# Kernel tuning notes

Hardware: AMD Instinct MI355X
Metric: run time of the kernel (lower is better)

Reference implementation:

```python
import jax, jax.numpy as jnp
import numpy as np

H, DH, C, K = 8, 128, 200, 15  # heads, head_dim, context_size, conv kernel
SCALE = DH ** -0.5
EPS = 1e-5


def layernorm(x, g, b):
    mu = jnp.mean(x, axis=-1, keepdims=True)
    var = jnp.mean(jnp.square(x - mu), axis=-1, keepdims=True)
    return (x - mu) * jax.lax.rsqrt(var + EPS) * g + b


def feedforward(x, ln_g, ln_b, up_w, up_b, down_w, down_b):
    h = layernorm(x, ln_g, ln_b)
    h = jax.nn.silu(h @ up_w + up_b)
    return h @ down_w + down_b


def attention(x, dist, ln_g, ln_b, wq, wkv, wo, wo_b, rel_emb):
    h = layernorm(x, ln_g, ln_b)
    b, f, d = h.shape
    nb = f // C  # num_features chosen divisible by context_size (no remainder path)
    q = (h @ wq).reshape(b, nb, C, H, DH).transpose(0, 1, 3, 2, 4)   # [b,nb,H,C,dh]
    kv = h @ wkv
    k, v = jnp.split(kv, 2, axis=-1)
    k = k.reshape(b, nb, C, H, DH).transpose(0, 1, 3, 2, 4)
    v = v.reshape(b, nb, C, H, DH).transpose(0, 1, 3, 2, 4)
    rel = rel_emb[dist]                                              # [C,C,dh]
    pos_attn = jnp.einsum('bnhid,ijd->bnhij', q, rel) * SCALE
    scores = jnp.einsum('bnhid,bnhjd->bnhij', q, k) * SCALE + pos_attn
    probs = jax.nn.softmax(scores, axis=-1)
    out = jnp.einsum('bnhij,bnhjd->bnhid', probs, v)
    out = out.transpose(0, 1, 3, 2, 4).reshape(b, f, H * DH)
    return out @ wo + wo_b


def conv_module(x, ln_g, ln_b, up_w, up_b, dw_w, bn_g, bn_b, bn_mean, bn_var, down_w, down_b):
    h = layernorm(x, ln_g, ln_b)
    h = h @ up_w + up_b                         # pointwise conv == linear; [b,L,2*inner]
    a, gate = jnp.split(h, 2, axis=-1)
    h = a * jax.nn.sigmoid(gate)                # GLU over channel dim
    h = h.transpose(0, 2, 1)                    # [b,inner,L]
    pad = K // 2
    h = jax.lax.conv_general_dilated(
        h, dw_w[:, None, :], window_strides=(1,), padding=[(pad, pad)],
        dimension_numbers=('NCH', 'OIH', 'NCH'), feature_group_count=h.shape[1])
    # BatchNorm1d in eval mode (running stats)
    h = (h - bn_mean[None, :, None]) * jax.lax.rsqrt(bn_var[None, :, None] + EPS)
    h = h * bn_g[None, :, None] + bn_b[None, :, None]
    h = jax.nn.silu(h)
    h = h.transpose(0, 2, 1) @ down_w + down_b  # [b,L,hidden]
    return h


def block_forward(x, attention_dists,
                  ff1_ln_g, ff1_ln_b, ff1_up_w, ff1_up_b, ff1_down_w, ff1_down_b,
                  attn_ln_g, attn_ln_b, wq, wkv, wo, wo_b, rel_emb,
                  conv_ln_g, conv_ln_b, conv_up_w, conv_up_b, dw_w,
                  bn_g, bn_b, bn_mean, bn_var, conv_down_w, conv_down_b,
                  ff2_ln_g, ff2_ln_b, ff2_up_w, ff2_up_b, ff2_down_w, ff2_down_b,
                  post_ln_g, post_ln_b):
    x = 0.5 * feedforward(x, ff1_ln_g, ff1_ln_b, ff1_up_w, ff1_up_b, ff1_down_w, ff1_down_b) + x
    x = attention(x, attention_dists, attn_ln_g, attn_ln_b, wq, wkv, wo, wo_b, rel_emb) + x
    x = conv_module(x, conv_ln_g, conv_ln_b, conv_up_w, conv_up_b, dw_w,
                    bn_g, bn_b, bn_mean, bn_var, conv_down_w, conv_down_b) + x
    x = 0.5 * feedforward(x, ff2_ln_g, ff2_ln_b, ff2_up_w, ff2_up_b, ff2_down_w, ff2_down_b) + x
    return layernorm(x, post_ln_g, post_ln_b)


def setup_inputs() -> dict:
    key = jax.random.key(0)
    ks = iter(jax.random.split(key, 40))
    d, dff, inner = 1024, 4096, 2048
    r = lambda shape, s=0.02: (jax.random.normal(next(ks), shape, jnp.float32) * s)
    inp = {
        'x': jax.random.normal(next(ks), (8, 2000, d), jnp.float32),
        'attention_dists': jax.random.randint(next(ks), (C, C), 0, 1025, jnp.int32),
        'ff1_ln_g': jnp.ones((d,)), 'ff1_ln_b': jnp.zeros((d,)),
        'ff1_up_w': r((d, dff)), 'ff1_up_b': jnp.zeros((dff,)),
        'ff1_down_w': r((dff, d)), 'ff1_down_b': jnp.zeros((d,)),
        'attn_ln_g': jnp.ones((d,)), 'attn_ln_b': jnp.zeros((d,)),
        'wq': r((d, H * DH)), 'wkv': r((d, 2 * H * DH)),
        'wo': r((H * DH, d)), 'wo_b': jnp.zeros((d,)),
        'rel_emb': r((2 * 512 + 1, DH)),
        'conv_ln_g': jnp.ones((d,)), 'conv_ln_b': jnp.zeros((d,)),
        'conv_up_w': r((d, 2 * inner)), 'conv_up_b': jnp.zeros((2 * inner,)),
        'dw_w': r((inner, K)),
        'bn_g': jnp.ones((inner,)), 'bn_b': jnp.zeros((inner,)),
        'bn_mean': r((inner,)), 'bn_var': jax.random.uniform(next(ks), (inner,), jnp.float32) + 0.5,
        'conv_down_w': r((inner, d)), 'conv_down_b': jnp.zeros((d,)),
        'ff2_ln_g': jnp.ones((d,)), 'ff2_ln_b': jnp.zeros((d,)),
        'ff2_up_w': r((d, dff)), 'ff2_up_b': jnp.zeros((dff,)),
        'ff2_down_w': r((dff, d)), 'ff2_down_b': jnp.zeros((d,)),
        'post_ln_g': jnp.ones((d,)), 'post_ln_b': jnp.zeros((d,)),
    }
    return inp


def reference(x, attention_dists,
              ff1_ln_g, ff1_ln_b, ff1_up_w, ff1_up_b, ff1_down_w, ff1_down_b,
              attn_ln_g, attn_ln_b, wq, wkv, wo, wo_b, rel_emb,
              conv_ln_g, conv_ln_b, conv_up_w, conv_up_b, dw_w,
              bn_g, bn_b, bn_mean, bn_var, conv_down_w, conv_down_b,
              ff2_ln_g, ff2_ln_b, ff2_up_w, ff2_up_b, ff2_down_w, ff2_down_b,
              post_ln_g, post_ln_b):
    return block_forward(x, attention_dists,
                         ff1_ln_g, ff1_ln_b, ff1_up_w, ff1_up_b, ff1_down_w, ff1_down_b,
                         attn_ln_g, attn_ln_b, wq, wkv, wo, wo_b, rel_emb,
                         conv_ln_g, conv_ln_b, conv_up_w, conv_up_b, dw_w,
                         bn_g, bn_b, bn_mean, bn_var, conv_down_w, conv_down_b,
                         ff2_ln_g, ff2_ln_b, ff2_up_w, ff2_up_b, ff2_down_w, ff2_down_b,
                         post_ln_g, post_ln_b)
```

## Files before the change

### kernel.cpp

```cpp
#include <hip/hip_runtime.h>

typedef unsigned short u16;
typedef unsigned int u32;
using short8 = __attribute__((ext_vector_type(8))) short;
using floatx4 = __attribute__((ext_vector_type(4))) float;

#define DMODEL 1024
#define DFF 4096
#define INNER 2048
#define DH 128
#define CTX 200
#define R_TOT 16000
#define ABN 40
#define AROWS (ABN * CTX)
#define AM (ABN * 8)
#define SCALE_Q 0.08838834764831845f

__device__ __forceinline__ u16 f2bf(float f) {
    union { float f; u32 u; } v; v.f = f;
    u32 r = v.u + 0x7FFFu + ((v.u >> 16) & 1u);
    return (u16)(r >> 16);
}
__device__ __forceinline__ float bf2f(u16 u) {
    union { u32 u; float f; } v; v.u = ((u32)u) << 16; return v.f;
}
__device__ __forceinline__ float sigmoidf_(float x) { return 1.f / (1.f + __expf(-x)); }

__device__ __forceinline__ void load_lds16(const void* g, void* l) {
    __builtin_amdgcn_global_load_lds((const __attribute__((address_space(1))) u32*)g,
                                     (__attribute__((address_space(3))) u32*)l, 16, 0, 0);
}

__device__ __forceinline__ void xcd_stripe_remap(int& bx, int& by) {
    const int gx = gridDim.x;
    const int gxs = gx >> 3;
    const int id = blockIdx.y * gx + blockIdx.x;
    const int xcd = id & 7;
    const int local = id >> 3;
    bx = xcd * gxs + (local % gxs);
    by = local / gxs;
}

template <int MODE>
__device__ __forceinline__ void epi_store(int r, int c, float v, int M, int ldc,
                                          const float* bias, float alpha, void* out,
                                          const float* resid) {
    if (r >= M) return;
    size_t idx = (size_t)r * ldc + c;
    float bb = bias ? bias[c] : 0.f;
    if (MODE == 0) {
        ((u16*)out)[idx] = f2bf(alpha * v + bb);
    } else if (MODE == 1) {
        float t = v + bb;
        ((u16*)out)[idx] = f2bf(t * sigmoidf_(t));
    } else {
        ((float*)out)[idx] = alpha * (v + bb) + resid[idx];
    }
}

template <int MODE>
__global__ __launch_bounds__(256, 4) void k_g(const u16* __restrict__ A, int lda,
                                              const u16* __restrict__ Bt, int ldb,
                                              const float* __restrict__ bias, float alpha,
                                              void* out, int ldc, const float* resid, int M,
                                              int N, int K) {
    __shared__ __align__(128) char lds[32768];
    int bx, by;
    xcd_stripe_remap(bx, by);
    const int row0 = bx * 128, col0 = by * 128;
    if (row0 >= M) return;
    const int lane = threadIdx.x & 63;
    const int wave = threadIdx.x >> 6;
    const int wrow = (wave >> 1) * 64;
    const int wcol = (wave & 1) * 64;
    const int lr = lane & 15;
    const int kg = lane >> 4;
    const int nt = K >> 6;

    const char* sA[4];
    const char* sB[4];
#pragma unroll
    for (int r = 0; r < 4; ++r) {
        int o = r * 4096 + wave * 1024 + lane * 16;
        int row = o >> 7;
        int srcb = (o & 127) ^ ((row & 7) << 4);
        int ga = row0 + row;
        ga = (ga < M) ? ga : M - 1;
        sA[r] = (const char*)A + (size_t)ga * ((size_t)lda * 2) + srcb;
        int gb = col0 + row;
        gb = (gb < N) ? gb : N - 1;
        sB[r] = (const char*)Bt + (size_t)gb * ((size_t)ldb * 2) + srcb;
    }
    floatx4 acc[4][4];
#pragma unroll
    for (int i = 0; i < 4; ++i)
#pragma unroll
        for (int j = 0; j < 4; ++j) acc[i][j] = (floatx4){0.f, 0.f, 0.f, 0.f};

    for (int t = 0; t < nt; ++t) {
        const int kb = t << 7;
#pragma unroll
        for (int r = 0; r < 4; ++r) {
            load_lds16(sA[r] + kb, lds + r * 4096 + wave * 1024);
            load_lds16(sB[r] + kb, lds + 16384 + r * 4096 + wave * 1024);
        }
        asm volatile("s_waitcnt vmcnt(0)" ::: "memory");
        __builtin_amdgcn_s_barrier();
#pragma unroll
        for (int ks = 0; ks < 2; ++ks) {
            short8 av[4], bv[4];
#pragma unroll
            for (int mi = 0; mi < 4; ++mi) {
                int row = wrow + mi * 16 + lr;
                int cb = (ks * 64 + kg * 16) ^ ((row & 7) << 4);
                av[mi] = *(const short8*)(lds + row * 128 + cb);
            }
#pragma unroll
            for (int ni = 0; ni < 4; ++ni) {
                int row = wcol + ni * 16 + lr;
                int cb = (ks * 64 + kg * 16) ^ ((row & 7) << 4);
                bv[ni] = *(const short8*)(lds + 16384 + row * 128 + cb);
            }
#pragma unroll
            for (int mi = 0; mi < 4; ++mi)
#pragma unroll
                for (int ni = 0; ni < 4; ++ni)
                    acc[mi][ni] = __builtin_amdgcn_mfma_f32_16x16x32_bf16(av[mi], bv[ni],
                                                                          acc[mi][ni], 0, 0, 0);
        }
        asm volatile("s_waitcnt lgkmcnt(0)" ::: "memory");
        __builtin_amdgcn_s_barrier();
    }
#pragma unroll
    for (int mi = 0; mi < 4; ++mi)
#pragma unroll
        for (int ni = 0; ni < 4; ++ni)
#pragma unroll
            for (int rr = 0; rr < 4; ++rr)
                epi_store<MODE>(row0 + wrow + mi * 16 + kg * 4 + rr, col0 + wcol + ni * 16 + lr,
                                acc[mi][ni][rr], M, ldc, bias, alpha, out, resid);
}

template <typename RowMap>
__device__ __forceinline__ void stage_tile_s(const char* __restrict__ src, RowMap rowoff,
                                             int nrows, int row0, int k0b, char* tile) {
    const int lane = threadIdx.x & 63;
    const int wave = threadIdx.x >> 6;
#pragma unroll
    for (int r = 0; r < 4; ++r) {
        int o = r * 4096 + wave * 1024 + lane * 16;
        int row = o >> 7;
        int srcb = (o & 127) ^ ((row & 7) << 4);
        int grow = row0 + row;
        grow = (grow < nrows) ? grow : (nrows - 1);
        load_lds16(src + rowoff(grow) + k0b + srcb, tile + r * 4096 + wave * 1024);
    }
}

template <typename RMA, typename RMB, typename Epi>
__device__ __forceinline__ void gemm_core_s(const char* __restrict__ A, RMA rma, int a_rows,
                                            const char* __restrict__ B, RMB rmb, int b_rows,
                                            int K, int row0, int col0, char* lds, Epi epi) {
    const int lane = threadIdx.x & 63;
    const int wave = threadIdx.x >> 6;
    const int wrow = (wave >> 1) * 64;
    const int wcol = (wave & 1) * 64;
    const int lr = lane & 15;
    const int kg = lane >> 4;
    const int nt = K >> 6;

    floatx4 acc[4][4];
#pragma unroll
    for (int i = 0; i < 4; ++i)
#pragma unroll
        for (int j = 0; j < 4; ++j) acc[i][j] = (floatx4){0.f, 0.f, 0.f, 0.f};

    for (int t = 0; t < nt; ++t) {
        const int kb = t << 7;
        stage_tile_s(A, rma, a_rows, row0, kb, lds);
        stage_tile_s(B, rmb, b_rows, col0, kb, lds + 16384);
        asm volatile("s_waitcnt vmcnt(0)" ::: "memory");
        __builtin_amdgcn_s_barrier();
#pragma unroll
        for (int ks = 0; ks < 2; ++ks) {
            short8 av[4], bv[4];
#pragma unroll
            for (int mi = 0; mi < 4; ++mi) {
                int row = wrow + mi * 16 + lr;
                int cb = (ks * 64 + kg * 16) ^ ((row & 7) << 4);
                av[mi] = *(const short8*)(lds + row * 128 + cb);
            }
#pragma unroll
            for (int ni = 0; ni < 4; ++ni) {
                int row = wcol + ni * 16 + lr;
                int cb = (ks * 64 + kg * 16) ^ ((row & 7) << 4);
                bv[ni] = *(const short8*)(lds + 16384 + row * 128 + cb);
            }
#pragma unroll
            for (int mi = 0; mi < 4; ++mi)
#pragma unroll
                for (int ni = 0; ni < 4; ++ni)
                    acc[mi][ni] = __builtin_amdgcn_mfma_f32_16x16x32_bf16(av[mi], bv[ni],
                                                                          acc[mi][ni], 0, 0, 0);
        }
        asm volatile("s_waitcnt lgkmcnt(0)" ::: "memory");
        __builtin_amdgcn_s_barrier();
    }
#pragma unroll
    for (int mi = 0; mi < 4; ++mi)
#pragma unroll
        for (int ni = 0; ni < 4; ++ni)
#pragma unroll
            for (int rr = 0; rr < 4; ++rr)
                epi(row0 + wrow + mi * 16 + kg * 4 + rr, col0 + wcol + ni * 16 + lr,
                    acc[mi][ni][rr]);
}

__global__ __launch_bounds__(256, 4) void k_qk(const u16* __restrict__ q,
                                               const u16* __restrict__ kvc,
                                               u16* __restrict__ sc, int bn0) {
    __shared__ __align__(128) char lds[32768];
    const int z = blockIdx.z, bnl = z >> 3, h = z & 7;
    const char* A = (const char*)(q + ((size_t)(bn0 + bnl) * CTX) * DMODEL + h * DH);
    const char* B = (const char*)(kvc + ((size_t)bnl * CTX) * (2 * DMODEL) + h * DH);
    u16* out = sc + (size_t)z * CTX * 256;
    gemm_core_s(A, [](int r) { return (size_t)r * (DMODEL * 2); }, CTX, B,
                [](int r) { return (size_t)r * (4 * DMODEL); }, CTX, DH, blockIdx.x * 128,
                blockIdx.y * 128, lds, [&](int r, int c, float v) {
                    if (r < CTX) out[(size_t)r * 256 + c] = f2bf(v);
                });
}

__global__ __launch_bounds__(256, 4) void k_pos(const u16* __restrict__ q,
                                                const u16* __restrict__ rel,
                                                u16* __restrict__ sc, int m0) {
    __shared__ __align__(128) char lds[32768];
    const int i = blockIdx.z;
    const char* B = (const char*)(rel + (size_t)i * CTX * DH);
    u16* out = sc + i * 256;
    gemm_core_s((const char*)q,
                [=](int r) {
                    int m = m0 + r;
                    return (size_t)(((m >> 3) * CTX + i) * DMODEL + (m & 7) * DH) * 2;
                },
                AM, B, [](int r) { return (size_t)r * (DH * 2); }, CTX, DH, blockIdx.x * 128,
                blockIdx.y * 128, lds, [&](int r, int c, float v) {
                    if (r < AM) {
                        size_t idx = (size_t)r * (CTX * 256) + c;
                        out[idx] = f2bf(bf2f(out[idx]) + v);
                    }
                });
}

__global__ __launch_bounds__(256, 4) void k_pv(const u16* __restrict__ P,
                                               const u16* __restrict__ vT,
                                               u16* __restrict__ attn, int bn0) {
    __shared__ __align__(128) char lds[32768];
    const int z = blockIdx.z;
    u16* out = attn + ((size_t)(bn0 + (z >> 3)) * CTX) * DMODEL + (z & 7) * DH;
    const char* A = (const char*)(P + (size_t)z * CTX * 256);
    const char* B = (const char*)(vT + (size_t)z * DH * 256);
    gemm_core_s(A, [](int r) { return (size_t)r * 512; }, CTX, B,
                [](int r) { return (size_t)r * 512; }, DH, 256, blockIdx.x * 128, 0, lds,
                [&](int r, int c, float v) {
                    if (r < CTX) out[(size_t)r * DMODEL + c] = f2bf(v);
                });
}

template <bool OUTF32>
__global__ __launch_bounds__(256) void k_ln(const float* __restrict__ x,
                                            const float* __restrict__ g,
                                            const float* __restrict__ b, void* __restrict__ out) {
    const int row = blockIdx.x, t = threadIdx.x, lane = t & 63, wv = t >> 6;
    const float4 v = ((const float4*)(x + (size_t)row * DMODEL))[t];
    float s = v.x + v.y + v.z + v.w;
    float q = v.x * v.x + v.y * v.y + v.z * v.z + v.w * v.w;
#pragma unroll
    for (int off = 32; off > 0; off >>= 1) { s += __shfl_down(s, off); q += __shfl_down(q, off); }
    __shared__ float rs_[4], rq_[4];
    if (lane == 0) { rs_[wv] = s; rq_[wv] = q; }
    __syncthreads();
    s = rs_[0] + rs_[1] + rs_[2] + rs_[3];
    q = rq_[0] + rq_[1] + rq_[2] + rq_[3];
    const float mu = s * (1.f / DMODEL);
    const float rstd = rsqrtf(q * (1.f / DMODEL) - mu * mu + 1e-5f);
    const float4 gv = ((const float4*)g)[t];
    const float4 bv = ((const float4*)b)[t];
    float o0 = (v.x - mu) * rstd * gv.x + bv.x;
    float o1 = (v.y - mu) * rstd * gv.y + bv.y;
    float o2 = (v.z - mu) * rstd * gv.z + bv.z;
    float o3 = (v.w - mu) * rstd * gv.w + bv.w;
    if (OUTF32) {
        ((float4*)out)[(size_t)row * 256 + t] = make_float4(o0, o1, o2, o3);
    } else {
        ushort4 r4;
        r4.x = f2bf(o0); r4.y = f2bf(o1); r4.z = f2bf(o2); r4.w = f2bf(o3);
        ((ushort4*)out)[(size_t)row * 256 + t] = r4;
    }
}

__global__ __launch_bounds__(256) void k_softmax(u16* __restrict__ sc) {
    const size_t row = blockIdx.x;
    const int t = threadIdx.x, lane = t & 63, wv = t >> 6;
    float v = (t < CTX) ? bf2f(sc[row * 256 + t]) : -3.0e38f;
    float m = v;
#pragma unroll
    for (int off = 32; off > 0; off >>= 1) m = fmaxf(m, __shfl_down(m, off));
    __shared__ float rm[4], rsum[4];
    if (lane == 0) rm[wv] = m;
    __syncthreads();
    m = fmaxf(fmaxf(rm[0], rm[1]), fmaxf(rm[2], rm[3]));
    float e = (t < CTX) ? __expf(v - m) : 0.f;
    float s = e;
#pragma unroll
    for (int off = 32; off > 0; off >>= 1) s += __shfl_down(s, off);
    if (lane == 0) rsum[wv] = s;
    __syncthreads();
    s = rsum[0] + rsum[1] + rsum[2] + rsum[3];
    sc[row * 256 + t] = f2bf(e / s);
}

__global__ __launch_bounds__(256) void k_glu(u16* __restrict__ mid) {
    const size_t r = blockIdx.x;
    const int c = threadIdx.x * 8;
    const short8 a8 = *(const short8*)(mid + r * 4096 + c);
    const short8 g8 = *(const short8*)(mid + r * 4096 + 2048 + c);
    short8 o8;
#pragma unroll
    for (int e = 0; e < 8; ++e) {
        float av = bf2f((u16)a8[e]), gg = bf2f((u16)g8[e]);
        o8[e] = (short)f2bf(av * sigmoidf_(gg));
    }
    *(short8*)(mid + r * 4096 + c) = o8;
}

__global__ __launch_bounds__(256) void k_dwconv(const u16* __restrict__ in,
                                                const float* __restrict__ w,
                                                const float* __restrict__ bng,
                                                const float* __restrict__ bnb,
                                                const float* __restrict__ bnm,
                                                const float* __restrict__ bnv,
                                                u16* __restrict__ out) {
    const int b = blockIdx.z, lt = blockIdx.x, cg = blockIdx.y;
    const int c = cg * 256 + threadIdx.x;
    const int l0 = lt * 16;
    __shared__ u16 s[30][256];
#pragma unroll
    for (int rr = 0; rr < 30; ++rr) {
        int l = l0 + rr - 7;
        u16 v = 0;
        if (l >= 0 && l < 2000) v = in[((size_t)b * 2000 + l) * 4096 + c];
        s[rr][threadIdx.x] = v;
    }
    __syncthreads();
    float wv[15];
#pragma unroll
    for (int k = 0; k < 15; ++k) wv[k] = w[c * 15 + k];
    const float sc = rsqrtf(bnv[c] + 1e-5f) * bng[c];
    const float mean = bnm[c], bb = bnb[c];
#pragma unroll
    for (int l = 0; l < 16; ++l) {
        float acc = 0.f;
#pragma unroll
        for (int k = 0; k < 15; ++k) acc += bf2f(s[l + k][threadIdx.x]) * wv[k];
        float h = (acc - mean) * sc + bb;
        h = h * sigmoidf_(h);
        out[((size_t)b * 2000 + l0 + l) * 4096 + c] = f2bf(h);
    }
}

__global__ __launch_bounds__(256) void k_wt(const float* __restrict__ w, u16* __restrict__ wt,
                                            int K, int N) {
    __shared__ float tile[32][33];
    const int k0 = blockIdx.x * 32, n0 = blockIdx.y * 32;
    const int tx = threadIdx.x & 31, ty = threadIdx.x >> 5;
#pragma unroll
    for (int i = 0; i < 32; i += 8) tile[ty + i][tx] = w[(size_t)(k0 + ty + i) * N + n0 + tx];
    __syncthreads();
#pragma unroll
    for (int i = 0; i < 32; i += 8)
        wt[(size_t)(n0 + ty + i) * K + k0 + tx] = f2bf(tile[tx][ty + i]);
}

__global__ void k_rel(const float* __restrict__ emb, const int* __restrict__ dist,
                      u16* __restrict__ rel) {
    const int bid = blockIdx.x;
    const int d = dist[bid];
    rel[(size_t)bid * DH + threadIdx.x] = f2bf(emb[(size_t)d * DH + threadIdx.x]);
}

__global__ __launch_bounds__(256) void k_vt(const u16* __restrict__ kvc, u16* __restrict__ vT) {
    __shared__ u16 t_[64 * 130];
    const int z = blockIdx.x, jt = blockIdx.y;
    const int bnl = z >> 3, h = z & 7;
    const int j0 = jt * 64;
    for (int idx = threadIdx.x; idx < 8192; idx += 256) {
        int j = idx >> 7, dh = idx & 127;
        int jj = j0 + j;
        u16 val = 0;
        if (jj < CTX) val = kvc[((size_t)(bnl * CTX + jj)) * (2 * DMODEL) + DMODEL + h * DH + dh];
        t_[j * 130 + dh] = val;
    }
    __syncthreads();
    for (int idx = threadIdx.x; idx < 8192; idx += 256) {
        int dh = idx >> 6, j = idx & 63;
        vT[((size_t)z * DH + dh) * 256 + j0 + j] = t_[j * 130 + dh];
    }
}

__global__ void k_fill(float* o, int n, float v) {
    int i = blockIdx.x * 256 + threadIdx.x;
    if (i < n) o[i] = v;
}

extern "C" void kernel_launch(void* const* d_in, const int* in_sizes, int n_in, void* d_out,
                              int out_size, void* d_ws, size_t ws_size, hipStream_t stream) {
    const float* x_in = (const float*)d_in[0];
    const int* dists = (const int*)d_in[1];
    const float* ff1_ln_g = (const float*)d_in[2];
    const float* ff1_ln_b = (const float*)d_in[3];
    const float* ff1_up_w = (const float*)d_in[4];
    const float* ff1_up_b = (const float*)d_in[5];
    const float* ff1_down_w = (const float*)d_in[6];
    const float* ff1_down_b = (const float*)d_in[7];
    const float* attn_ln_g = (const float*)d_in[8];
    const float* attn_ln_b = (const float*)d_in[9];
    const float* wq = (const float*)d_in[10];
    const float* wkv = (const float*)d_in[11];
    const float* wo = (const float*)d_in[12];
    const float* wo_b = (const float*)d_in[13];
    const float* rel_emb = (const float*)d_in[14];
    const float* conv_ln_g = (const float*)d_in[15];
    const float* conv_ln_b = (const float*)d_in[16];
    const float* conv_up_w = (const float*)d_in[17];
    const float* conv_up_b = (const float*)d_in[18];
    const float* dw_w = (const float*)d_in[19];
    const float* bn_g = (const float*)d_in[20];
    const float* bn_b = (const float*)d_in[21];
    const float* bn_mean = (const float*)d_in[22];
    const float* bn_var = (const float*)d_in[23];
    const float* conv_down_w = (const float*)d_in[24];
    const float* conv_down_b = (const float*)d_in[25];
    const float* ff2_ln_g = (const float*)d_in[26];
    const float* ff2_ln_b = (const float*)d_in[27];
    const float* ff2_up_w = (const float*)d_in[28];
    const float* ff2_up_b = (const float*)d_in[29];
    const float* ff2_down_w = (const float*)d_in[30];
    const float* ff2_down_b = (const float*)d_in[31];
    const float* post_ln_g = (const float*)d_in[32];
    const float* post_ln_b = (const float*)d_in[33];

    char* W = (char*)d_ws;
    size_t off = 0;
    auto alloc = [&](size_t bytes) {
        char* p = W + off;
        off += (bytes + 255) & ~(size_t)255;
        return (u16*)p;
    };
    u16* slot = alloc((size_t)4096 * 1024 * 2);
    u16* ln_buf = alloc((size_t)R_TOT * DMODEL * 2);
    u16* arena = alloc((size_t)R_TOT * DFF * 2);
    u16* mid = arena;
    u16* rel_bf = arena;
    u16* bufA = rel_bf + (size_t)CTX * CTX * DH;
    u16* bufB = bufA + (size_t)AROWS * 2 * DMODEL;
    u16* smid = bufB + (size_t)R_TOT * DMODEL;
    u16* vT = smid + (size_t)AM * CTX * 256;
    float* xs = (float*)d_out;

    if (ws_size < off) {
        k_fill<<<(out_size + 255) / 256, 256, 0, stream>>>((float*)d_out, out_size, 31337.f);
        return;
    }

    auto WT = [&](const float* s, int K, int N) {
        k_wt<<<dim3(K / 32, N / 32), 256, 0, stream>>>(s, slot, K, N);
    };

    const dim3 gUP(128, 32);
    const dim3 gSQ(128, 8);
    const dim3 gKV(64, 16);

    auto ff_block = [&](const float* lng, const float* lnb, const float* upw, const float* upb,
                        const float* dnw, const float* dnb, const float* resid,
                        const float* xsrc) {
        k_ln<false><<<R_TOT, 256, 0, stream>>>(xsrc, lng, lnb, ln_buf);
        WT(upw, 1024, 4096);
        k_g<1><<<gUP, 256, 0, stream>>>(ln_buf, DMODEL, slot, DMODEL, upb, 1.f, mid, DFF,
                                        nullptr, R_TOT, DFF, DMODEL);
        WT(dnw, 4096, 1024);
        k_g<2><<<gSQ, 256, 0, stream>>>(mid, DFF, slot, DFF, dnb, 0.5f, xs, DMODEL, resid,
                                        R_TOT, DMODEL, DFF);
    };

    ff_block(ff1_ln_g, ff1_ln_b, ff1_up_w, ff1_up_b, ff1_down_w, ff1_down_b, x_in, x_in);

    k_ln<false><<<R_TOT, 256, 0, stream>>>(xs, attn_ln_g, attn_ln_b, ln_buf);
    k_rel<<<CTX * CTX, 128, 0, stream>>>(rel_emb, dists, rel_bf);
    WT(wq, 1024, 1024);
    k_g<0><<<gSQ, 256, 0, stream>>>(ln_buf, DMODEL, slot, DMODEL, nullptr, SCALE_Q, bufB,
                                    DMODEL, nullptr, R_TOT, DMODEL, DMODEL);
    WT(wkv, 1024, 2048);
    for (int h = 0; h < 2; ++h) {
        const int bn0 = h * ABN, m0 = bn0 * 8;
        const u16* lnc = ln_buf + (size_t)bn0 * CTX * DMODEL;
        k_g<0><<<gKV, 256, 0, stream>>>(lnc, DMODEL, slot, DMODEL, nullptr, 1.f, bufA,
                                        2 * DMODEL, nullptr, AROWS, 2 * DMODEL, DMODEL);
        k_vt<<<dim3(AM, 4), 256, 0, stream>>>(bufA, vT);
        k_qk<<<dim3(2, 2, AM), 256, 0, stream>>>(bufB, bufA, smid, bn0);
        k_pos<<<dim3(3, 2, CTX), 256, 0, stream>>>(bufB, rel_bf, smid, m0);
        k_softmax<<<AM * CTX, 256, 0, stream>>>(smid);
        k_pv<<<dim3(2, 1, AM), 256, 0, stream>>>(smid, vT, bufB, bn0);
    }
    WT(wo, 1024, 1024);
    k_g<2><<<gSQ, 256, 0, stream>>>(bufB, DMODEL, slot, DMODEL, wo_b, 1.f, xs, DMODEL, xs,
                                    R_TOT, DMODEL, DMODEL);

    k_ln<false><<<R_TOT, 256, 0, stream>>>(xs, conv_ln_g, conv_ln_b, ln_buf);
    WT(conv_up_w, 1024, 4096);
    k_g<0><<<gUP, 256, 0, stream>>>(ln_buf, DMODEL, slot, DMODEL, conv_up_b, 1.f, mid, DFF,
                                    nullptr, R_TOT, DFF, DMODEL);
    k_glu<<<R_TOT, 256, 0, stream>>>(mid);
    k_dwconv<<<dim3(125, 8, 8), 256, 0, stream>>>(mid, dw_w, bn_g, bn_b, bn_mean, bn_var,
                                                  mid + INNER);
    WT(conv_down_w, 2048, 1024);
    k_g<2><<<gSQ, 256, 0, stream>>>(mid + INNER, DFF, slot, INNER, conv_down_b, 1.f, xs,
                                    DMODEL, xs, R_TOT, DMODEL, INNER);

    ff_block(ff2_ln_g, ff2_ln_b, ff2_up_w, ff2_up_b, ff2_down_w, ff2_down_b, xs, xs);

    k_ln<true><<<R_TOT, 256, 0, stream>>>(xs, post_ln_g, post_ln_b, d_out);
}
```

Before: 1.672 ms.

## Replace GEMM with 256x256-tile double-buffered 512-thread kernel

Replaces the 128x128-tile, single-buffered GEMM with a 256x256-tile, 8-wave kernel. It double-buffers 128 KB of LDS so the next K-tile's global-to-LDS loads overlap the current tile's MFMAs, and raises wave priority around the MFMA bursts. The larger tile improves operand reuse per byte loaded. The cost is one block per CU and much higher register use from the 8x4 accumulators. With fewer blocks, the 16000x1024 GEMMs get 256 tiles and the KV GEMMs get small grids, which risks poor CU coverage and tail effects.

Result: slower. 1.841 ms (+10.2%).

```diff
diff --git a/kernel.cpp b/kernel.cpp
--- a/kernel.cpp
+++ b/kernel.cpp
@@ -59,20 +59,20 @@
 }
 
 template <int MODE>
-__global__ __launch_bounds__(256, 4) void k_g(const u16* __restrict__ A, int lda,
-                                              const u16* __restrict__ Bt, int ldb,
-                                              const float* __restrict__ bias, float alpha,
-                                              void* out, int ldc, const float* resid, int M,
-                                              int N, int K) {
-    __shared__ __align__(128) char lds[32768];
+__global__ __launch_bounds__(512, 1) void k_g2(const u16* __restrict__ A, int lda,
+                                               const u16* __restrict__ Bt, int ldb,
+                                               const float* __restrict__ bias, float alpha,
+                                               void* out, int ldc, const float* resid, int M,
+                                               int N, int K) {
+    __shared__ __align__(128) char lds[131072];
     int bx, by;
     xcd_stripe_remap(bx, by);
-    const int row0 = bx * 128, col0 = by * 128;
+    const int row0 = bx * 256, col0 = by * 256;
     if (row0 >= M) return;
     const int lane = threadIdx.x & 63;
     const int wave = threadIdx.x >> 6;
-    const int wrow = (wave >> 1) * 64;
-    const int wcol = (wave & 1) * 64;
+    const int wrow = (wave >> 2) * 128;
+    const int wcol = (wave & 3) * 64;
     const int lr = lane & 15;
     const int kg = lane >> 4;
     const int nt = K >> 6;
@@ -81,7 +81,7 @@
     const char* sB[4];
 #pragma unroll
     for (int r = 0; r < 4; ++r) {
-        int o = r * 4096 + wave * 1024 + lane * 16;
+        int o = r * 8192 + wave * 1024 + lane * 16;
         int row = o >> 7;
         int srcb = (o & 127) ^ ((row & 7) << 4);
         int ga = row0 + row;
@@ -91,48 +91,83 @@
         gb = (gb < N) ? gb : N - 1;
         sB[r] = (const char*)Bt + (size_t)gb * ((size_t)ldb * 2) + srcb;
     }
-    floatx4 acc[4][4];
-#pragma unroll
-    for (int i = 0; i < 4; ++i)
+    floatx4 acc[8][4];
+#pragma unroll
+    for (int i = 0; i < 8; ++i)
 #pragma unroll
         for (int j = 0; j < 4; ++j) acc[i][j] = (floatx4){0.f, 0.f, 0.f, 0.f};
 
+#pragma unroll
+    for (int r = 0; r < 4; ++r) load_lds16(sA[r], lds + r * 8192 + wave * 1024);
+#pragma unroll
+    for (int r = 0; r < 4; ++r) load_lds16(sB[r], lds + 32768 + r * 8192 + wave * 1024);
+
     for (int t = 0; t < nt; ++t) {
-        const int kb = t << 7;
-#pragma unroll
-        for (int r = 0; r < 4; ++r) {
-            load_lds16(sA[r] + kb, lds + r * 4096 + wave * 1024);
-            load_lds16(sB[r] + kb, lds + 16384 + r * 4096 + wave * 1024);
-        }
-        asm volatile("s_waitcnt vmcnt(0)" ::: "memory");
+        char* cur = lds + (t & 1) * 65536;
+        char* nxt = lds + ((t + 1) & 1) * 65536;
+        const int kb = (t + 1) << 7;
+        if (t + 1 < nt) {
+#pragma unroll
+            for (int r = 0; r < 4; ++r) load_lds16(sA[r] + kb, nxt + r * 8192 + wave * 1024);
+            asm volatile("s_waitcnt vmcnt(4)" ::: "memory");
+        } else {
+            asm volatile("s_waitcnt vmcnt(0)" ::: "memory");
+        }
         __builtin_amdgcn_s_barrier();
-#pragma unroll
-        for (int ks = 0; ks < 2; ++ks) {
-            short8 av[4], bv[4];
-#pragma unroll
-            for (int mi = 0; mi < 4; ++mi) {
-                int row = wrow + mi * 16 + lr;
-                int cb = (ks * 64 + kg * 16) ^ ((row & 7) << 4);
-                av[mi] = *(const short8*)(lds + row * 128 + cb);
-            }
-#pragma unroll
-            for (int ni = 0; ni < 4; ++ni) {
-                int row = wcol + ni * 16 + lr;
-                int cb = (ks * 64 + kg * 16) ^ ((row & 7) << 4);
-                bv[ni] = *(const short8*)(lds + 16384 + row * 128 + cb);
-            }
-#pragma unroll
-            for (int mi = 0; mi < 4; ++mi)
-#pragma unroll
-                for (int ni = 0; ni < 4; ++ni)
-                    acc[mi][ni] = __builtin_amdgcn_mfma_f32_16x16x32_bf16(av[mi], bv[ni],
-                                                                          acc[mi][ni], 0, 0, 0);
+        short8 av[8], bv[4];
+#pragma unroll
+        for (int mi = 0; mi < 8; ++mi) {
+            int row = wrow + mi * 16 + lr;
+            int cb = (kg * 16) ^ ((row & 7) << 4);
+            av[mi] = *(const short8*)(cur + row * 128 + cb);
+        }
+#pragma unroll
+        for (int ni = 0; ni < 4; ++ni) {
+            int row = wcol + ni * 16 + lr;
+            int cb = (kg * 16) ^ ((row & 7) << 4);
+            bv[ni] = *(const short8*)(cur + 32768 + row * 128 + cb);
         }
         asm volatile("s_waitcnt lgkmcnt(0)" ::: "memory");
+        __builtin_amdgcn_sched_barrier(0);
+        __builtin_amdgcn_s_setprio(1);
+#pragma unroll
+        for (int mi = 0; mi < 8; ++mi)
+#pragma unroll
+            for (int ni = 0; ni < 4; ++ni)
+                acc[mi][ni] =
+                    __builtin_amdgcn_mfma_f32_16x16x32_bf16(av[mi], bv[ni], acc[mi][ni], 0, 0, 0);
+        __builtin_amdgcn_s_setprio(0);
+        if (t + 1 < nt) {
+#pragma unroll
+            for (int r = 0; r < 4; ++r)
+                load_lds16(sB[r] + kb, nxt + 32768 + r * 8192 + wave * 1024);
+        }
+#pragma unroll
+        for (int mi = 0; mi < 8; ++mi) {
+            int row = wrow + mi * 16 + lr;
+            int cb = (64 + kg * 16) ^ ((row & 7) << 4);
+            av[mi] = *(const short8*)(cur + row * 128 + cb);
+        }
+#pragma unroll
+        for (int ni = 0; ni < 4; ++ni) {
+            int row = wcol + ni * 16 + lr;
+            int cb = (64 + kg * 16) ^ ((row & 7) << 4);
+            bv[ni] = *(const short8*)(cur + 32768 + row * 128 + cb);
+        }
+        asm volatile("s_waitcnt lgkmcnt(0)" ::: "memory");
+        __builtin_amdgcn_sched_barrier(0);
+        __builtin_amdgcn_s_setprio(1);
+#pragma unroll
+        for (int mi = 0; mi < 8; ++mi)
+#pragma unroll
+            for (int ni = 0; ni < 4; ++ni)
+                acc[mi][ni] =
+                    __builtin_amdgcn_mfma_f32_16x16x32_bf16(av[mi], bv[ni], acc[mi][ni], 0, 0, 0);
+        __builtin_amdgcn_s_setprio(0);
         __builtin_amdgcn_s_barrier();
     }
 #pragma unroll
-    for (int mi = 0; mi < 4; ++mi)
+    for (int mi = 0; mi < 8; ++mi)
 #pragma unroll
         for (int ni = 0; ni < 4; ++ni)
 #pragma unroll
@@ -477,20 +512,20 @@
         k_wt<<<dim3(K / 32, N / 32), 256, 0, stream>>>(s, slot, K, N);
     };
 
-    const dim3 gUP(128, 32);
-    const dim3 gSQ(128, 8);
-    const dim3 gKV(64, 16);
+    const dim3 gUP(64, 16);
+    const dim3 gSQ(64, 4);
+    const dim3 gKV(32, 8);
 
     auto ff_block = [&](const float* lng, const float* lnb, const float* upw, const float* upb,
                         const float* dnw, const float* dnb, const float* resid,
                         const float* xsrc) {
         k_ln<false><<<R_TOT, 256, 0, stream>>>(xsrc, lng, lnb, ln_buf);
         WT(upw, 1024, 4096);
-        k_g<1><<<gUP, 256, 0, stream>>>(ln_buf, DMODEL, slot, DMODEL, upb, 1.f, mid, DFF,
-                                        nullptr, R_TOT, DFF, DMODEL);
+        k_g2<1><<<gUP, 512, 0, stream>>>(ln_buf, DMODEL, slot, DMODEL, upb, 1.f, mid, DFF,
+                                         nullptr, R_TOT, DFF, DMODEL);
         WT(dnw, 4096, 1024);
-        k_g<2><<<gSQ, 256, 0, stream>>>(mid, DFF, slot, DFF, dnb, 0.5f, xs, DMODEL, resid,
-                                        R_TOT, DMODEL, DFF);
+        k_g2<2><<<gSQ, 512, 0, stream>>>(mid, DFF, slot, DFF, dnb, 0.5f, xs, DMODEL, resid,
+                                         R_TOT, DMODEL, DFF);
     };
 
     ff_block(ff1_ln_g, ff1_ln_b, ff1_up_w, ff1_up_b, ff1_down_w, ff1_down_b, x_in, x_in);
@@ -498,14 +533,14 @@
     k_ln<false><<<R_TOT, 256, 0, stream>>>(xs, attn_ln_g, attn_ln_b, ln_buf);
     k_rel<<<CTX * CTX, 128, 0, stream>>>(rel_emb, dists, rel_bf);
     WT(wq, 1024, 1024);
-    k_g<0><<<gSQ, 256, 0, stream>>>(ln_buf, DMODEL, slot, DMODEL, nullptr, SCALE_Q, bufB,
-                                    DMODEL, nullptr, R_TOT, DMODEL, DMODEL);
+    k_g2<0><<<gSQ, 512, 0, stream>>>(ln_buf, DMODEL, slot, DMODEL, nullptr, SCALE_Q, bufB,
+                                     DMODEL, nullptr, R_TOT, DMODEL, DMODEL);
     WT(wkv, 1024, 2048);
     for (int h = 0; h < 2; ++h) {
         const int bn0 = h * ABN, m0 = bn0 * 8;
         const u16* lnc = ln_buf + (size_t)bn0 * CTX * DMODEL;
-        k_g<0><<<gKV, 256, 0, stream>>>(lnc, DMODEL, slot, DMODEL, nullptr, 1.f, bufA,
-                                        2 * DMODEL, nullptr, AROWS, 2 * DMODEL, DMODEL);
+        k_g2<0><<<gKV, 512, 0, stream>>>(lnc, DMODEL, slot, DMODEL, nullptr, 1.f, bufA,
+                                         2 * DMODEL, nullptr, AROWS, 2 * DMODEL, DMODEL);
         k_vt<<<dim3(AM, 4), 256, 0, stream>>>(bufA, vT);
         k_qk<<<dim3(2, 2, AM), 256, 0, stream>>>(bufB, bufA, smid, bn0);
         k_pos<<<dim3(3, 2, CTX), 256, 0, stream>>>(bufB, rel_bf, smid, m0);
@@ -513,19 +548,19 @@
         k_pv<<<dim3(2, 1, AM), 256, 0, stream>>>(smid, vT, bufB, bn0);
     }
     WT(wo, 1024, 1024);
-    k_g<2><<<gSQ, 256, 0, stream>>>(bufB, DMODEL, slot, DMODEL, wo_b, 1.f, xs, DMODEL, xs,
-                                    R_TOT, DMODEL, DMODEL);
+    k_g2<2><<<gSQ, 512, 0, stream>>>(bufB, DMODEL, slot, DMODEL, wo_b, 1.f, xs, DMODEL, xs,
+                                     R_TOT, DMODEL, DMODEL);
 
     k_ln<false><<<R_TOT, 256, 0, stream>>>(xs, conv_ln_g, conv_ln_b, ln_buf);
     WT(conv_up_w, 1024, 4096);
-    k_g<0><<<gUP, 256, 0, stream>>>(ln_buf, DMODEL, slot, DMODEL, conv_up_b, 1.f, mid, DFF,
-                                    nullptr, R_TOT, DFF, DMODEL);
+    k_g2<0><<<gUP, 512, 0, stream>>>(ln_buf, DMODEL, slot, DMODEL, conv_up_b, 1.f, mid, DFF,
+                                     nullptr, R_TOT, DFF, DMODEL);
     k_glu<<<R_TOT, 256, 0, stream>>>(mid);
     k_dwconv<<<dim3(125, 8, 8), 256, 0, stream>>>(mid, dw_w, bn_g, bn_b, bn_mean, bn_var,
                                                   mid + INNER);
     WT(conv_down_w, 2048, 1024);
-    k_g<2><<<gSQ, 256, 0, stream>>>(mid + INNER, DFF, slot, INNER, conv_down_b, 1.f, xs,
-                                    DMODEL, xs, R_TOT, DMODEL, INNER);
+    k_g2<2><<<gSQ, 512, 0, stream>>>(mid + INNER, DFF, slot, INNER, conv_down_b, 1.f, xs,
+                                     DMODEL, xs, R_TOT, DMODEL, INNER);
 
     ff_block(ff2_ln_g, ff2_ln_b, ff2_up_w, ff2_up_b, ff2_down_w, ff2_down_b, xs, xs);
 
```
